# Kernel tuning notes

Hardware: AMD Instinct MI355X
Metric: run time of the kernel (lower is better)

## Reference

```python
import jax, jax.numpy as jnp
import numpy as np

QMAX = 255.0  # bit=8 unsigned activation range


def ste_round(x):
    # straight-through round: exact integer rounding in fwd, identity grad
    return x + jax.lax.stop_gradient(jnp.round(x) - x)


def conv3x3(x, w, stride=1):
    return jax.lax.conv_general_dilated(
        x, w, window_strides=(stride, stride), padding=((1, 1), (1, 1)),
        dimension_numbers=('NCHW', 'OIHW', 'NCHW'))


def setup_inputs() -> dict:
    key = jax.random.key(0)
    k0, k1, k2 = jax.random.split(key, 3)
    N, C, H, W = 64, 256, 28, 28
    # uint8 activations and int8 (symmetric) weights, stored as integer-valued fp32
    x = jax.random.randint(k0, (N, C, H, W), 0, 256).astype(jnp.float32)
    w1 = jax.random.randint(k1, (C, C, 3, 3), -128, 128).astype(jnp.float32)
    w2 = jax.random.randint(k2, (C, C, 3, 3), -128, 128).astype(jnp.float32)
    f = jnp.float32
    return dict(
        x=x, w1=w1, w2=w2,
        s_x=f(0.05), z_x=f(128.0),
        s_w1=f(0.01), s_conv1=f(0.08), z_conv1=f(120.0),
        s_w2=f(0.01), s_conv2=f(0.07), z_conv2=f(130.0),
        s_add=f(0.09), z_add=f(125.0))


def qconv(x_q, w_q, s_in, z_in, s_w, s_out, z_out, stride=1):
    # integer-arithmetic conv: sum((x - z_in) * w) then requantize
    acc = conv3x3(x_q - z_in, w_q, stride)
    M = s_in * s_w / s_out  # per-cluster requant multiplier (cluster 0)
    return jnp.clip(ste_round(M * acc) + z_out, 0.0, QMAX)


def qadd(a, s_a, z_a, b, s_b, z_b, s_out, z_out):
    # fused dequant of both branches + residual add + requant
    y = (s_a / s_out) * (a - z_a) + (s_b / s_out) * (b - z_b)
    return jnp.clip(ste_round(y) + z_out, 0.0, QMAX)


def reference(x, w1, w2, s_x, z_x, s_w1, s_conv1, z_conv1,
              s_w2, s_conv2, z_conv2, s_add, z_add):
    out = qconv(x, w1, s_x, z_x, s_w1, s_conv1, z_conv1)          # conv1
    out = qconv(out, w2, s_conv1, z_conv1, s_w2, s_conv2, z_conv2)  # conv2
    return qadd(x, s_x, z_x, out, s_conv2, z_conv2, s_add, z_add)   # shortcut
```

## Files before the change

### kernel.cpp

```cpp
#include <hip/hip_runtime.h>
#include <stdint.h>

#define HWP 784
#define NPOS 50176
#define PLN ((size_t)NPOS * 64)
#define PAD_OFF 47616

typedef int   int4v   __attribute__((ext_vector_type(4)));
typedef int   int16v  __attribute__((ext_vector_type(16)));
typedef float float4v __attribute__((ext_vector_type(4)));
using as1_cv = const __attribute__((address_space(1))) void;
using as3_v  = __attribute__((address_space(3))) void;

__global__ __launch_bounds__(256) void k_nhwc(const float* __restrict__ x,
                                              int8_t* __restrict__ x8) {
    __shared__ int lA[256 * 15];
    __shared__ __align__(16) int lB[56 * 68];
    const int tid = threadIdx.x;
    const int P0 = blockIdx.x * 56;
    const int n = P0 / HWP;
    const int hw0 = P0 % HWP;
    const float* xb = x + (size_t)n * 256 * HWP + hw0;
#pragma unroll
    for (int k = 0; k < 14; ++k) {
        int e = tid + k * 256;
        int c = e / 14, pq = e % 14;
        float4v v = *(const float4v*)(xb + (size_t)c * HWP + pq * 4);
        int b0 = ((int)v[0] - 128) & 255;
        int b1 = ((int)v[1] - 128) & 255;
        int b2 = ((int)v[2] - 128) & 255;
        int b3 = ((int)v[3] - 128) & 255;
        lA[c * 15 + pq] = b0 | (b1 << 8) | (b2 << 16) | (b3 << 24);
    }
    __syncthreads();
#pragma unroll
    for (int k = 0; k < 4; ++k) {
        int u = tid + k * 256;
        if (u < 896) {
            int cg = u / 14, pq = u % 14;
            int d0 = lA[(cg * 4 + 0) * 15 + pq];
            int d1 = lA[(cg * 4 + 1) * 15 + pq];
            int d2 = lA[(cg * 4 + 2) * 15 + pq];
            int d3 = lA[(cg * 4 + 3) * 15 + pq];
#pragma unroll
            for (int j = 0; j < 4; ++j) {
                int sh = j * 8;
                int o = ((d0 >> sh) & 255) | (((d1 >> sh) & 255) << 8)
                      | (((d2 >> sh) & 255) << 16) | (((d3 >> sh) & 255) << 24);
                lB[(pq * 4 + j) * 68 + cg] = o;
            }
        }
    }
    __syncthreads();
#pragma unroll
    for (int k = 0; k < 4; ++k) {
        int ch = tid + k * 256;
        if (ch < 896) {
            int g = ch / 224, rem = ch % 224;
            int pos = rem >> 2, c4 = rem & 3;
            int4v val = *(const int4v*)&lB[pos * 68 + g * 16 + c4 * 4];
            *(int4v*)(x8 + (size_t)g * PLN + (size_t)(P0 + pos) * 64 + c4 * 16) = val;
        }
    }
}

__global__ __launch_bounds__(256) void k_w_prep(const float* __restrict__ wa,
                                                const float* __restrict__ wb,
                                                int8_t* __restrict__ w8a,
                                                int8_t* __restrict__ w8b,
                                                int* __restrict__ wsa,
                                                int* __restrict__ wsb) {
    __shared__ int red[256];
    const int which = blockIdx.x >> 8;
    const int oc = blockIdx.x & 255;
    const float* w = which ? wb : wa;
    int8_t* w8 = which ? w8b : w8a;
    int* wsum = which ? wsb : wsa;
    const int t = threadIdx.x;
    const float* src = w + (size_t)oc * 2304 + (size_t)t * 9;
    const int g = oc >> 5;
    const int l = ((t >> 4) & 1) * 32 + (oc & 31);
    const int j = t & 15;
    const int s2 = (t >> 5) & 1;
    const int kb = t >> 6;
    int acc = 0;
#pragma unroll
    for (int tap = 0; tap < 9; ++tap) {
        int wv = (int)src[tap];
        acc += wv;
        int oo = ((((tap * 4 + kb) * 2 + s2) * 8 + g) * 64 + l) * 16 + j;
        w8[oo] = (int8_t)wv;
    }
    red[t] = acc;
    __syncthreads();
    for (int st = 128; st > 0; st >>= 1) {
        if (t < st) red[t] += red[t + st];
        __syncthreads();
    }
    if (t == 0) wsum[oc] = red[0];
}

template<bool FUSED>
__global__ __launch_bounds__(256, 3) void k_qconv_t(const int8_t* __restrict__ in8,
        const int8_t* __restrict__ w8, const int* __restrict__ wsum,
        const float* __restrict__ s_in_p, const float* __restrict__ s_w_p,
        const float* __restrict__ s_out_p, const float* __restrict__ z_in_p,
        const float* __restrict__ z_out_p, int8_t* __restrict__ out8,
        const int8_t* __restrict__ x8, const float* __restrict__ sxp,
        const float* __restrict__ zxp, const float* __restrict__ sap,
        const float* __restrict__ zap, float* __restrict__ outf) {
    __shared__ __align__(16) int8_t slab[47872];
    const int tid = threadIdx.x;
    const int lane = tid & 63;
    const int half = lane >> 5;
    const int wv = tid >> 6;
    const int wq = wv >> 1;
    const int wo = wv & 1;
    const int p0 = blockIdx.x * 128;
    const int gB = blockIdx.y * 128;

#pragma unroll
    for (int k = 0; k < 12; ++k) {
        int chunkid = tid + k * 256;
        if (chunkid < 2976) {
            int q = chunkid >> 4;
            int cs = chunkid & 15;
            int cg = cs ^ (q & 15);
            int qg = p0 - 29 + q;
            qg = qg < 0 ? 0 : (qg > NPOS - 1 ? NPOS - 1 : qg);
            const int8_t* src = in8 + (size_t)(cg >> 2) * PLN
                                    + (size_t)qg * 64 + (cg & 3) * 16;
            __builtin_amdgcn_global_load_lds((as1_cv*)src,
                                             (as3_v*)&slab[chunkid * 16], 16, 0, 0);
        }
    }

    const int zi = (int)z_in_p[0] - 128;
    const int spl = (zi & 0xff) * 0x01010101;
    if (tid < 16) {
        int4v pv; pv[0] = spl; pv[1] = spl; pv[2] = spl; pv[3] = spl;
        *(int4v*)&slab[PAD_OFF + tid * 16] = pv;
    }

    int rowpos[2], ph[2], pw[2];
#pragma unroll
    for (int mt = 0; mt < 2; ++mt) {
        rowpos[mt] = wq * 64 + mt * 32 + (lane & 31);
        int p = p0 + rowpos[mt];
        int hw = p % HWP;
        ph[mt] = hw / 28;
        pw[mt] = hw % 28;
    }
    int abz[9][2];
#pragma unroll
    for (int tap = 0; tap < 9; ++tap) {
        const int dh = tap / 3 - 1;
        const int dw = tap % 3 - 1;
#pragma unroll
        for (int mt = 0; mt < 2; ++mt) {
            int q = rowpos[mt] + dh * 28 + dw + 29;
            bool ok = ((unsigned)(ph[mt] + dh) < 28u) & ((unsigned)(pw[mt] + dw) < 28u);
            int base = ok ? (q << 8) : PAD_OFF;
            abz[tap][mt] = base ^ ((q & 15) << 4) ^ (half << 4);
        }
    }

    int16v acc[2][2];
#pragma unroll
    for (int mt = 0; mt < 2; ++mt)
#pragma unroll
        for (int nt = 0; nt < 2; ++nt)
#pragma unroll
            for (int r = 0; r < 16; ++r) acc[mt][nt][r] = 0;

    const int gg0 = blockIdx.y * 4 + wo * 2;
    const int8_t* wlane = w8 + gg0 * 1024 + lane * 16;

    int4v areg[2][2][2];
    int4v breg[3][2][2];

#define LOADB(u, slot)                                                      \
    {   const int8_t* wb_ = wlane + (size_t)(u) * 16384;                    \
        breg[slot][0][0] = *(const int4v*)(wb_);                            \
        breg[slot][1][0] = *(const int4v*)(wb_ + 1024);                     \
        breg[slot][0][1] = *(const int4v*)(wb_ + 8192);                     \
        breg[slot][1][1] = *(const int4v*)(wb_ + 9216); }
#define LOADA(u, slot)                                                      \
    {   const int tap_ = (u) >> 2, kb_ = (u) & 3;                           \
        areg[slot][0][0] = *(const int4v*)&slab[abz[tap_][0] ^ ((kb_*4+0)<<4)]; \
        areg[slot][0][1] = *(const int4v*)&slab[abz[tap_][0] ^ ((kb_*4+2)<<4)]; \
        areg[slot][1][0] = *(const int4v*)&slab[abz[tap_][1] ^ ((kb_*4+0)<<4)]; \
        areg[slot][1][1] = *(const int4v*)&slab[abz[tap_][1] ^ ((kb_*4+2)<<4)]; }

    LOADB(0, 0);
    LOADB(1, 1);

    __syncthreads();

    LOADA(0, 0);
#pragma unroll
    for (int u = 0; u < 36; ++u) {
        if (u < 34) LOADB(u + 2, (u + 2) % 3);
        if (u < 35) LOADA(u + 1, (u + 1) & 1);
        const int sl = u & 1;
        const int bs = u % 3;
#pragma unroll
        for (int s = 0; s < 2; ++s)
#pragma unroll
            for (int mt = 0; mt < 2; ++mt)
#pragma unroll
                for (int nt = 0; nt < 2; ++nt)
                    acc[mt][nt] = __builtin_amdgcn_mfma_i32_32x32x32_i8(
                        areg[sl][mt][s], breg[bs][nt][s], acc[mt][nt], 0, 0, 0);
    }
#undef LOADA
#undef LOADB

    const float Mf = s_in_p[0] * s_w_p[0] / s_out_p[0];
    const float zof = z_out_p[0];
    const int zoffi = 128 - (int)z_in_p[0];
    const int plane = blockIdx.y * 2 + wo;

    if (!FUSED) {
        __syncthreads();
        int8_t* tpb = slab + wv * 5120;
#pragma unroll
        for (int mt = 0; mt < 2; ++mt)
#pragma unroll
            for (int nt = 0; nt < 2; ++nt) {
                int oc = gB + wo * 64 + nt * 32 + (lane & 31);
                int corr = zoffi * wsum[oc];
#pragma unroll
                for (int r = 0; r < 16; ++r) {
                    int prow = (r & 3) + 8 * (r >> 2) + 4 * half;
                    int pl = mt * 32 + prow;
                    float q = rintf(Mf * (float)(acc[mt][nt][r] + corr)) + zof;
                    q = fminf(fmaxf(q, 0.0f), 255.0f);
                    tpb[pl * 80 + nt * 32 + (lane & 31)] = (int8_t)((int)q - 128);
                }
            }
        int8_t* o8p = out8 + (size_t)plane * PLN + (size_t)(p0 + wq * 64 + lane) * 64;
        const int8_t* rowp = tpb + lane * 80;
#pragma unroll
        for (int k = 0; k < 4; ++k)
            *(int4v*)(o8p + k * 16) = *(const int4v*)(rowp + k * 16);
    } else {
        const float ra = sxp[0] / sap[0];
        const float rb = s_out_p[0] / sap[0];
        const float zx = zxp[0];
        const float z2 = z_out_p[0];
        const float za = zap[0];
        __syncthreads();
        float* tp = (float*)slab + wv * 2080;
        const int pl = lane & 31;
#pragma unroll
        for (int mt = 0; mt < 2; ++mt) {
#pragma unroll
            for (int nt = 0; nt < 2; ++nt) {
                int oc = gB + wo * 64 + nt * 32 + (lane & 31);
                int corr = zoffi * wsum[oc];
#pragma unroll
                for (int r = 0; r < 16; ++r) {
                    int prow = (r & 3) + 8 * (r >> 2) + 4 * half;
                    float q2 = rintf(Mf * (float)(acc[mt][nt][r] + corr)) + zof;
                    q2 = fminf(fmaxf(q2, 0.0f), 255.0f);
                    tp[prow * 65 + nt * 32 + (lane & 31)] = q2;
                }
            }
            const int pglob = p0 + wq * 64 + mt * 32 + pl;
            const int n = pglob / HWP;
            const int hwo = pglob % HWP;
            const int8_t* x8p = x8 + (size_t)plane * PLN + (size_t)pglob * 64 + half * 32;
            int4v r0 = *(const int4v*)x8p;
            int4v r1 = *(const int4v*)(x8p + 16);
            int xb[8];
            xb[0] = r0[0]; xb[1] = r0[1]; xb[2] = r0[2]; xb[3] = r0[3];
            xb[4] = r1[0]; xb[5] = r1[1]; xb[6] = r1[2]; xb[7] = r1[3];
            float* obase = outf + ((size_t)(n * 256 + gB + wo * 64 + half * 32)) * HWP + hwo;
#pragma unroll
            for (int j = 0; j < 32; ++j) {
                int bv = (xb[j >> 2] >> ((j & 3) * 8)) & 255;
                int xval = (int)(int8_t)bv + 128;
                float q2 = tp[pl * 65 + half * 32 + j];
                float y = ra * ((float)xval - zx) + rb * (q2 - z2);
                float qf = rintf(y) + za;
                qf = fminf(fmaxf(qf, 0.0f), 255.0f);
                obase[(size_t)j * HWP] = qf;
            }
        }
    }
}

extern "C" void kernel_launch(void* const* d_in, const int* in_sizes, int n_in,
                              void* d_out, int out_size, void* d_ws, size_t ws_size,
                              hipStream_t stream) {
    (void)in_sizes; (void)n_in; (void)out_size; (void)ws_size;
    const float* x    = (const float*)d_in[0];
    const float* w1   = (const float*)d_in[1];
    const float* w2   = (const float*)d_in[2];
    const float* s_x  = (const float*)d_in[3];
    const float* z_x  = (const float*)d_in[4];
    const float* s_w1 = (const float*)d_in[5];
    const float* s_c1 = (const float*)d_in[6];
    const float* z_c1 = (const float*)d_in[7];
    const float* s_w2 = (const float*)d_in[8];
    const float* s_c2 = (const float*)d_in[9];
    const float* z_c2 = (const float*)d_in[10];
    const float* s_ad = (const float*)d_in[11];
    const float* z_ad = (const float*)d_in[12];
    float* out = (float*)d_out;

    int8_t* ws    = (int8_t*)d_ws;
    int8_t* x8    = ws;
    int8_t* o1    = ws + 12845056;
    int8_t* w8a   = ws + 25690112;
    int8_t* w8b   = ws + 26279936;
    int*    wsum1 = (int*)(ws + 26869760);
    int*    wsum2 = (int*)(ws + 26870784);

    k_nhwc<<<896, 256, 0, stream>>>(x, x8);
    k_w_prep<<<512, 256, 0, stream>>>(w1, w2, w8a, w8b, wsum1, wsum2);
    k_qconv_t<false><<<dim3(392, 2), 256, 0, stream>>>(x8, w8a, wsum1,
        s_x, s_w1, s_c1, z_x, z_c1, o1,
        nullptr, nullptr, nullptr, nullptr, nullptr, nullptr);
    k_qconv_t<true><<<dim3(392, 2), 256, 0, stream>>>(o1, w8b, wsum2,
        s_c1, s_w2, s_c2, z_c1, z_c2, nullptr,
        x8, s_x, z_x, s_ad, z_ad, out);
}
```

Baseline: 212.8 us.

## Retile qconv to 64 positions x 256 channels per block, drop register prefetch

Each block of the int8 MFMA conv now covers 64 output positions and all 256 output channels, with the four waves splitting the channel dimension. Before, blocks covered 128 positions and 128 channels on a 2D grid. The input slab in LDS shrinks, which allows a launch bound of 4 blocks per CU, and the per-tap A-address table and the triple-buffered register prefetch of A/B operands are removed in favour of loads issued inline. The aim is higher occupancy with fewer registers and each input slab reused across all output channels. The cost is more halo reloads per position and less explicit latency hiding inside the MFMA loop.

```diff
diff --git a/kernel.cpp b/kernel.cpp
--- a/kernel.cpp
+++ b/kernel.cpp
@@ -4,7 +4,7 @@
 #define HWP 784
 #define NPOS 50176
 #define PLN ((size_t)NPOS * 64)
-#define PAD_OFF 47616
+#define PAD_OFF 31232
 
 typedef int   int4v   __attribute__((ext_vector_type(4)));
 typedef int   int16v  __attribute__((ext_vector_type(16)));
@@ -101,7 +101,7 @@
 }
 
 template<bool FUSED>
-__global__ __launch_bounds__(256, 3) void k_qconv_t(const int8_t* __restrict__ in8,
+__global__ __launch_bounds__(256, 4) void k_qconv_t(const int8_t* __restrict__ in8,
         const int8_t* __restrict__ w8, const int* __restrict__ wsum,
         const float* __restrict__ s_in_p, const float* __restrict__ s_w_p,
         const float* __restrict__ s_out_p, const float* __restrict__ z_in_p,
@@ -109,20 +109,17 @@
         const int8_t* __restrict__ x8, const float* __restrict__ sxp,
         const float* __restrict__ zxp, const float* __restrict__ sap,
         const float* __restrict__ zap, float* __restrict__ outf) {
-    __shared__ __align__(16) int8_t slab[47872];
+    __shared__ __align__(16) int8_t slab[33280];
     const int tid = threadIdx.x;
     const int lane = tid & 63;
     const int half = lane >> 5;
     const int wv = tid >> 6;
-    const int wq = wv >> 1;
-    const int wo = wv & 1;
-    const int p0 = blockIdx.x * 128;
-    const int gB = blockIdx.y * 128;
-
-#pragma unroll
-    for (int k = 0; k < 12; ++k) {
+    const int p0 = blockIdx.x * 64;
+
+#pragma unroll
+    for (int k = 0; k < 8; ++k) {
         int chunkid = tid + k * 256;
-        if (chunkid < 2976) {
+        if (chunkid < 1952) {
             int q = chunkid >> 4;
             int cs = chunkid & 15;
             int cg = cs ^ (q & 15);
@@ -145,65 +142,45 @@
     int rowpos[2], ph[2], pw[2];
 #pragma unroll
     for (int mt = 0; mt < 2; ++mt) {
-        rowpos[mt] = wq * 64 + mt * 32 + (lane & 31);
+        rowpos[mt] = mt * 32 + (lane & 31);
         int p = p0 + rowpos[mt];
         int hw = p % HWP;
         ph[mt] = hw / 28;
         pw[mt] = hw % 28;
     }
-    int abz[9][2];
-#pragma unroll
-    for (int tap = 0; tap < 9; ++tap) {
+
+    int16v acc[2][2];
+#pragma unroll
+    for (int mt = 0; mt < 2; ++mt)
+#pragma unroll
+        for (int nt = 0; nt < 2; ++nt)
+#pragma unroll
+            for (int r = 0; r < 16; ++r) acc[mt][nt][r] = 0;
+
+    const int8_t* wlane = w8 + wv * 2048 + lane * 16;
+
+    __syncthreads();
+
+#pragma unroll
+    for (int u = 0; u < 36; ++u) {
+        const int tap = u >> 2, kb = u & 3;
         const int dh = tap / 3 - 1;
         const int dw = tap % 3 - 1;
+        const int8_t* wb_ = wlane + (size_t)u * 16384;
+        int4v b[2][2];
+        b[0][0] = *(const int4v*)(wb_);
+        b[1][0] = *(const int4v*)(wb_ + 1024);
+        b[0][1] = *(const int4v*)(wb_ + 8192);
+        b[1][1] = *(const int4v*)(wb_ + 9216);
+        int4v a[2][2];
 #pragma unroll
         for (int mt = 0; mt < 2; ++mt) {
             int q = rowpos[mt] + dh * 28 + dw + 29;
             bool ok = ((unsigned)(ph[mt] + dh) < 28u) & ((unsigned)(pw[mt] + dw) < 28u);
-            int base = ok ? (q << 8) : PAD_OFF;
-            abz[tap][mt] = base ^ ((q & 15) << 4) ^ (half << 4);
-        }
-    }
-
-    int16v acc[2][2];
-#pragma unroll
-    for (int mt = 0; mt < 2; ++mt)
-#pragma unroll
-        for (int nt = 0; nt < 2; ++nt)
-#pragma unroll
-            for (int r = 0; r < 16; ++r) acc[mt][nt][r] = 0;
-
-    const int gg0 = blockIdx.y * 4 + wo * 2;
-    const int8_t* wlane = w8 + gg0 * 1024 + lane * 16;
-
-    int4v areg[2][2][2];
-    int4v breg[3][2][2];
-
-#define LOADB(u, slot)                                                      \
-    {   const int8_t* wb_ = wlane + (size_t)(u) * 16384;                    \
-        breg[slot][0][0] = *(const int4v*)(wb_);                            \
-        breg[slot][1][0] = *(const int4v*)(wb_ + 1024);                     \
-        breg[slot][0][1] = *(const int4v*)(wb_ + 8192);                     \
-        breg[slot][1][1] = *(const int4v*)(wb_ + 9216); }
-#define LOADA(u, slot)                                                      \
-    {   const int tap_ = (u) >> 2, kb_ = (u) & 3;                           \
-        areg[slot][0][0] = *(const int4v*)&slab[abz[tap_][0] ^ ((kb_*4+0)<<4)]; \
-        areg[slot][0][1] = *(const int4v*)&slab[abz[tap_][0] ^ ((kb_*4+2)<<4)]; \
-        areg[slot][1][0] = *(const int4v*)&slab[abz[tap_][1] ^ ((kb_*4+0)<<4)]; \
-        areg[slot][1][1] = *(const int4v*)&slab[abz[tap_][1] ^ ((kb_*4+2)<<4)]; }
-
-    LOADB(0, 0);
-    LOADB(1, 1);
-
-    __syncthreads();
-
-    LOADA(0, 0);
-#pragma unroll
-    for (int u = 0; u < 36; ++u) {
-        if (u < 34) LOADB(u + 2, (u + 2) % 3);
-        if (u < 35) LOADA(u + 1, (u + 1) & 1);
-        const int sl = u & 1;
-        const int bs = u % 3;
+            int ab = (ok ? (q << 8) : PAD_OFF) ^ ((q & 15) << 4) ^ (half << 4);
+            a[mt][0] = *(const int4v*)&slab[ab ^ ((kb * 4 + 0) << 4)];
+            a[mt][1] = *(const int4v*)&slab[ab ^ ((kb * 4 + 2) << 4)];
+        }
 #pragma unroll
         for (int s = 0; s < 2; ++s)
 #pragma unroll
@@ -211,15 +188,12 @@
 #pragma unroll
                 for (int nt = 0; nt < 2; ++nt)
                     acc[mt][nt] = __builtin_amdgcn_mfma_i32_32x32x32_i8(
-                        areg[sl][mt][s], breg[bs][nt][s], acc[mt][nt], 0, 0, 0);
-    }
-#undef LOADA
-#undef LOADB
+                        a[mt][s], b[nt][s], acc[mt][nt], 0, 0, 0);
+    }
 
     const float Mf = s_in_p[0] * s_w_p[0] / s_out_p[0];
     const float zof = z_out_p[0];
     const int zoffi = 128 - (int)z_in_p[0];
-    const int plane = blockIdx.y * 2 + wo;
 
     if (!FUSED) {
         __syncthreads();
@@ -228,7 +202,7 @@
         for (int mt = 0; mt < 2; ++mt)
 #pragma unroll
             for (int nt = 0; nt < 2; ++nt) {
-                int oc = gB + wo * 64 + nt * 32 + (lane & 31);
+                int oc = wv * 64 + nt * 32 + (lane & 31);
                 int corr = zoffi * wsum[oc];
 #pragma unroll
                 for (int r = 0; r < 16; ++r) {
@@ -239,7 +213,7 @@
                     tpb[pl * 80 + nt * 32 + (lane & 31)] = (int8_t)((int)q - 128);
                 }
             }
-        int8_t* o8p = out8 + (size_t)plane * PLN + (size_t)(p0 + wq * 64 + lane) * 64;
+        int8_t* o8p = out8 + (size_t)wv * PLN + (size_t)(p0 + lane) * 64;
         const int8_t* rowp = tpb + lane * 80;
 #pragma unroll
         for (int k = 0; k < 4; ++k)
@@ -257,7 +231,7 @@
         for (int mt = 0; mt < 2; ++mt) {
 #pragma unroll
             for (int nt = 0; nt < 2; ++nt) {
-                int oc = gB + wo * 64 + nt * 32 + (lane & 31);
+                int oc = wv * 64 + nt * 32 + (lane & 31);
                 int corr = zoffi * wsum[oc];
 #pragma unroll
                 for (int r = 0; r < 16; ++r) {
@@ -267,16 +241,16 @@
                     tp[prow * 65 + nt * 32 + (lane & 31)] = q2;
                 }
             }
-            const int pglob = p0 + wq * 64 + mt * 32 + pl;
+            const int pglob = p0 + mt * 32 + pl;
             const int n = pglob / HWP;
             const int hwo = pglob % HWP;
-            const int8_t* x8p = x8 + (size_t)plane * PLN + (size_t)pglob * 64 + half * 32;
+            const int8_t* x8p = x8 + (size_t)wv * PLN + (size_t)pglob * 64 + half * 32;
             int4v r0 = *(const int4v*)x8p;
             int4v r1 = *(const int4v*)(x8p + 16);
             int xb[8];
             xb[0] = r0[0]; xb[1] = r0[1]; xb[2] = r0[2]; xb[3] = r0[3];
             xb[4] = r1[0]; xb[5] = r1[1]; xb[6] = r1[2]; xb[7] = r1[3];
-            float* obase = outf + ((size_t)(n * 256 + gB + wo * 64 + half * 32)) * HWP + hwo;
+            float* obase = outf + ((size_t)(n * 256 + wv * 64 + half * 32)) * HWP + hwo;
 #pragma unroll
             for (int j = 0; j < 32; ++j) {
                 int bv = (xb[j >> 2] >> ((j & 3) * 8)) & 255;
@@ -320,10 +294,10 @@
 
     k_nhwc<<<896, 256, 0, stream>>>(x, x8);
     k_w_prep<<<512, 256, 0, stream>>>(w1, w2, w8a, w8b, wsum1, wsum2);
-    k_qconv_t<false><<<dim3(392, 2), 256, 0, stream>>>(x8, w8a, wsum1,
+    k_qconv_t<false><<<784, 256, 0, stream>>>(x8, w8a, wsum1,
         s_x, s_w1, s_c1, z_x, z_c1, o1,
         nullptr, nullptr, nullptr, nullptr, nullptr, nullptr);
-    k_qconv_t<true><<<dim3(392, 2), 256, 0, stream>>>(o1, w8b, wsum2,
+    k_qconv_t<true><<<784, 256, 0, stream>>>(o1, w8b, wsum2,
         s_c1, s_w2, s_c2, z_c1, z_c2, nullptr,
         x8, s_x, z_x, s_ad, z_ad, out);
 }
```

Result: no change. 210.0 us (-1.3%).
